# Optimization experiments

Hardware: AMD Instinct MI355X
Metric: run time of the kernel (lower is better)

## Reference

```python
import jax, jax.numpy as jnp
import numpy as np

B, C, N, IC = 4, 64, 4096, 32  # batch, in_channels(=g_channels), nodes, inter_channels


def setup_inputs() -> dict:
    key = jax.random.key(0)
    ks = jax.random.split(key, 8)
    s_c = (2.0 / C) ** 0.5   # kaiming-ish scales
    s_i = (2.0 / C) ** 0.5
    x = jax.random.normal(ks[0], (B, C, N), dtype=jnp.float32)
    g_w = jax.random.normal(ks[1], (C, C), dtype=jnp.float32) * s_c      # g: 1x1 conv (out=C, in=C)
    g_b = jnp.zeros((C,), dtype=jnp.float32)
    theta_w = jax.random.normal(ks[2], (IC, C), dtype=jnp.float32) * s_i  # theta: (out=IC, in=C)
    theta_b = jnp.zeros((IC,), dtype=jnp.float32)
    phi_w = jax.random.normal(ks[3], (IC, C), dtype=jnp.float32) * s_i
    phi_b = jnp.zeros((IC,), dtype=jnp.float32)
    cp_w = jax.random.normal(ks[4], (2 * IC,), dtype=jnp.float32) * (2.0 / (2 * IC)) ** 0.5  # concat_project 1x1 conv, no bias
    C_k = jnp.zeros((N, N), dtype=jnp.float32)  # learned adjacency bias, init zeros
    return {"x": x, "g_w": g_w, "g_b": g_b, "theta_w": theta_w, "theta_b": theta_b,
            "phi_w": phi_w, "phi_b": phi_b, "cp_w": cp_w, "C_k": C_k}


def reference(x, g_w, g_b, theta_w, theta_b, phi_w, phi_b, cp_w, C_k):
    # 1x1 convs are plain GEMMs over the node dim
    g_x = jnp.einsum('oc,bcn->bno', g_w, x) + g_b            # (B, N, C)
    th = jnp.einsum('oc,bcn->bon', theta_w, x) + theta_b[:, None]  # (B, IC, N)
    ph = jnp.einsum('oc,bcn->bon', phi_w, x) + phi_b[:, None]      # (B, IC, N)
    # concat_project on [theta_i ; phi_j] with a 1x1 conv is algebraically an outer sum:
    # f[b,i,j] = w_th . theta[b,:,i] + w_ph . phi[b,:,j]
    a = jnp.einsum('c,bcn->bn', cp_w[:IC], th)  # (B, N)
    p = jnp.einsum('c,bcn->bn', cp_w[IC:], ph)  # (B, N)
    f = a[:, :, None] + p[:, None, :]           # (B, N, N)
    attention = jax.nn.softmax(jax.nn.leaky_relu(f, negative_slope=0.2), axis=-1) + C_k
    y = jnp.einsum('bij,bjo->boi', attention, g_x)  # (B, C, N)
    return y
```

## Files before the change

kernel.cpp:

```cpp
#include <hip/hip_runtime.h>


#define B  4
#define C  64
#define N  4096
#define IC 32
#define NS 4104
#define NR 4097
#define MAGIC 0x13572468
#define CKQ 1048576

#define OFF_FLAG   248
#define OFF_A      256
#define OFF_P      (OFF_A + B*N)
#define OFF_Q      (OFF_P + B*N)
#define OFF_PERM   (OFF_Q + B*N)
#define OFF_PRES   (OFF_PERM + B*N)
#define OFF_SUFS   (OFF_PRES + B*NS)
#define OFF_S1     (OFF_SUFS + B*NS)
#define OFF_S2     (OFF_S1 + B*64*64)
#define OFF_GX     (OFF_S2 + B*64*64)
#define OFF_PREG   (OFF_GX + B*N*64)
#define OFF_SUFG   (OFF_PREG + B*NR*64)

#define CK_NZ(v) ((v.x != 0.f) | (v.y != 0.f) | (v.z != 0.f) | (v.w != 0.f))

__global__ __launch_bounds__(256) void k1_gx(
    const float* __restrict__ x, const float* __restrict__ g_w,
    const float* __restrict__ g_b, const float* __restrict__ theta_w,
    const float* __restrict__ theta_b, const float* __restrict__ phi_w,
    const float* __restrict__ phi_b, const float* __restrict__ cp_w,
    const float* __restrict__ Ck, float* __restrict__ ws) {
  __shared__ float gwT[C * C];
  __shared__ float xl[C * 16];
  __shared__ float lu[C], lv[C], cst[2];
  const int tid = threadIdx.x;
  const int b = blockIdx.x >> 8;
  const int n0 = (blockIdx.x & 255) << 4;
  const float4* c4 = (const float4*)Ck;
  float4 ck0, ck1, ck2, ck3;
  {
    int idx = (blockIdx.x << 8) + tid;
    ck0 = c4[idx]; ck1 = c4[idx + 262144];
    ck2 = c4[idx + 524288]; ck3 = c4[idx + 786432];
  }
  for (int idx = tid; idx < C * C; idx += 256) {
    int o = idx >> 6, cc = idx & 63;
    gwT[cc * C + o] = g_w[idx];
  }
  for (int idx = tid; idx < C * 16; idx += 256) {
    int cc = idx >> 4, nn = idx & 15;
    xl[idx] = x[(size_t)((b << 6) + cc) * N + n0 + nn];
  }
  if (tid < 64) {
    float u = 0.f;
    for (int k = 0; k < IC; ++k) u += cp_w[k] * theta_w[k * C + tid];
    lu[tid] = u;
  } else if (tid < 128) {
    int c = tid - 64;
    float v = 0.f;
    for (int k = 0; k < IC; ++k) v += cp_w[IC + k] * phi_w[k * C + c];
    lv[c] = v;
  } else if (tid == 128) {
    float ca = 0.f, cp2 = 0.f;
    for (int k = 0; k < IC; ++k) { ca += cp_w[k] * theta_b[k]; cp2 += cp_w[IC + k] * phi_b[k]; }
    cst[0] = ca; cst[1] = cp2;
  }
  __syncthreads();
  if (tid < 16) {
    float au = cst[0], pu = cst[1];
    for (int cc = 0; cc < C; ++cc) {
      float xv = xl[cc * 16 + tid];
      au += lu[cc] * xv;
      pu += lv[cc] * xv;
    }
    ws[OFF_A + (b << 12) + n0 + tid] = au;
    ws[OFF_P + (b << 12) + n0 + tid] = pu;
  }
  const int o = tid & 63, g4 = tid >> 6;
  float bb = g_b[o];
  float acc0 = bb, acc1 = bb, acc2 = bb, acc3 = bb;
  for (int cc = 0; cc < C; ++cc) {
    float gv = gwT[cc * C + o];
    const float* xr = &xl[cc * 16 + (g4 << 2)];
    acc0 += gv * xr[0]; acc1 += gv * xr[1]; acc2 += gv * xr[2]; acc3 += gv * xr[3];
  }
  float* gx = ws + OFF_GX + (size_t)((b << 12) + n0 + (g4 << 2)) * C + o;
  gx[0] = acc0; gx[64] = acc1; gx[128] = acc2; gx[192] = acc3;
  bool nz = CK_NZ(ck0) | CK_NZ(ck1) | CK_NZ(ck2) | CK_NZ(ck3);
  if (__any(nz) && (tid & 63) == 0)
    atomicExch((int*)ws + OFF_FLAG, MAGIC);
}

__global__ __launch_bounds__(1024) void k2_rank(const float* __restrict__ Ck,
                                                float* __restrict__ ws) {
  __shared__ float lp[N];
  __shared__ int partials[32][33];
  const int tid = threadIdx.x;
  const int b = blockIdx.x >> 7;
  const int rg = blockIdx.x & 127;
  const float4* c4 = (const float4*)Ck + CKQ;
  float4 ck0, ck1;
  {
    int idx = (blockIdx.x << 10) + tid;
    ck0 = c4[idx]; ck1 = c4[idx + 524288];
  }
  const float* p = ws + OFF_P + b * N;
  ((float4*)lp)[tid] = ((const float4*)p)[tid];
  const int row = tid & 31, chunk = tid >> 5;
  const int i = (rg << 5) + row;
  __syncthreads();
  const float my = lp[i];
  const int c0 = chunk << 7;
  const float4* lp4 = (const float4*)(lp + c0);
  int r0 = 0, r1 = 0, r2 = 0, r3 = 0;
  for (int j = 0; j < 32; ++j) {
    float4 v = lp4[j];
    int k = c0 + (j << 2);
    r0 += (v.x < my) || (v.x == my && (k + 0) < i);
    r1 += (v.y < my) || (v.y == my && (k + 1) < i);
    r2 += (v.z < my) || (v.z == my && (k + 2) < i);
    r3 += (v.w < my) || (v.w == my && (k + 3) < i);
  }
  partials[row][chunk] = (r0 + r1) + (r2 + r3);
  __syncthreads();
  if (tid < 32) {
    int rank = 0;
#pragma unroll
    for (int c = 0; c < 32; ++c) rank += partials[tid][c];
    const int ii = (rg << 5) + tid;
    ws[OFF_Q + (b << 12) + rank] = lp[ii];
    ((int*)ws)[OFF_PERM + (b << 12) + rank] = ii;
  }
  bool nz = CK_NZ(ck0) | CK_NZ(ck1);
  if (__any(nz) && (tid & 63) == 0)
    atomicExch((int*)ws + OFF_FLAG, MAGIC);
}

__global__ __launch_bounds__(1024) void k3_scan_chunks(const float* __restrict__ Ck,
                                                       float* __restrict__ ws) {
  __shared__ float sA[1024], sB[1024];
  const int tid = threadIdx.x;
  const int bid = blockIdx.x;
  const float4* c4 = (const float4*)Ck + 2 * CKQ;
  float4 ck0 = {0.f,0.f,0.f,0.f}, ck1 = ck0, ck2 = ck0, ck3 = ck0;
  {
    int idx = (bid << 10) + tid;
    if (idx < CKQ) ck0 = c4[idx];  idx += 266240;
    if (idx < CKQ) ck1 = c4[idx];  idx += 266240;
    if (idx < CKQ) ck2 = c4[idx];  idx += 266240;
    if (idx < CKQ) ck3 = c4[idx];
  }
  if (bid < B) {
    const int b = bid;
    float* wt2 = sA;
    float* wt1 = sA + 16;
    float* wo2 = sA + 32;
    float* wo1 = sA + 49;
    const float* q = ws + OFF_Q + b * N;
    const float4 qv4 = ((const float4*)q)[tid];
    float e1r[4], e2r[4];
    e2r[0] = expf(0.2f * qv4.x); e1r[0] = expf(qv4.x);
    e2r[1] = expf(0.2f * qv4.y); e1r[1] = expf(qv4.y);
    e2r[2] = expf(0.2f * qv4.z); e1r[2] = expf(qv4.z);
    e2r[3] = expf(0.2f * qv4.w); e1r[3] = expf(qv4.w);
    float s2 = e2r[0] + e2r[1] + e2r[2] + e2r[3];
    float s1 = e1r[0] + e1r[1] + e1r[2] + e1r[3];
    const int lane = tid & 63, wave = tid >> 6;
    float x2 = s2, x1 = s1;
    for (int off = 1; off < 64; off <<= 1) {
      float t2 = __shfl_up(x2, off, 64);
      float t1 = __shfl_up(x1, off, 64);
      if (lane >= off) { x2 += t2; x1 += t1; }
    }
    if (lane == 63) { wt2[wave] = x2; wt1[wave] = x1; }
    __syncthreads();
    if (wave == 0 && lane < 17) {
      float a2 = 0.f, a1 = 0.f;
      for (int w = 0; w < 16; ++w) {
        if (w < lane) { a2 += wt2[w]; a1 += wt1[w]; }
      }
      wo2[lane] = a2; wo1[lane] = a1;
    }
    __syncthreads();
    const float excl2 = wo2[wave] + (x2 - s2);
    const float incl1 = wo1[wave] + x1;
    const float tot1 = wo1[16];
    float* PreS = ws + OFF_PRES + b * NS;
    float* SufS = ws + OFF_SUFS + b * NS;
    const int base = tid << 2;
    float run = excl2;
#pragma unroll
    for (int j = 0; j < 4; ++j) { PreS[base + j] = run; run += e2r[j]; }
    if (tid == 1023) PreS[N] = run;
    run = tot1 - incl1;
#pragma unroll
    for (int j = 3; j >= 0; --j) { run += e1r[j]; SufS[base + j] = run; }
    if (tid == 1023) SufS[N] = 0.f;
  } else {
    const int b2 = bid - B;
    const int b = b2 >> 6, c = b2 & 63;
    const int o = tid & 63, kk = tid >> 6;
    const float* q = ws + OFF_Q + b * N;
    const int* perm = (const int*)ws + OFF_PERM + b * N;
    const float* gx = ws + OFF_GX + ((size_t)b << 18);
    float p1 = 0.f, p2 = 0.f;
    const int k0 = (c << 6) + (kk << 2);
    for (int r = 0; r < 4; ++r) {
      int k = k0 + r;
      float qv = q[k];
      float g = gx[((size_t)perm[k] << 6) + o];
      p1 += expf(qv) * g;
      p2 += expf(0.2f * qv) * g;
    }
    sA[(kk << 6) + o] = p2;
    sB[(kk << 6) + o] = p1;
    __syncthreads();
    if (tid < 64) {
      float t2 = 0.f, t1 = 0.f;
#pragma unroll
      for (int g = 0; g < 16; ++g) { t2 += sA[(g << 6) + o]; t1 += sB[(g << 6) + o]; }
      ws[OFF_S2 + (size_t)(((b << 6) + c) << 6) + o] = t2;
      ws[OFF_S1 + (size_t)(((b << 6) + c) << 6) + o] = t1;
    }
  }
  bool nz = CK_NZ(ck0) | CK_NZ(ck1) | CK_NZ(ck2) | CK_NZ(ck3);
  if (__any(nz) && (tid & 63) == 0)
    atomicExch((int*)ws + OFF_FLAG, MAGIC);
}

__global__ __launch_bounds__(1024) void k4_prefix(const float* __restrict__ Ck,
                                                  float* __restrict__ ws) {
  __shared__ float sA[1024], sB[1024];
  const int tid = threadIdx.x;
  const int b = blockIdx.x >> 6, c = blockIdx.x & 63;
  const int o = tid & 63, kk = tid >> 6;
  const float4* c4 = (const float4*)Ck + 3 * CKQ;
  float4 ck0, ck1, ck2, ck3;
  {
    int idx = (blockIdx.x << 10) + tid;
    ck0 = c4[idx]; ck1 = c4[idx + 262144];
    ck2 = c4[idx + 524288]; ck3 = c4[idx + 786432];
  }
  float offp = 0.f, offs = 0.f;
  {
    const float* S1 = ws + OFF_S1 + ((size_t)b << 12);
    const float* S2 = ws + OFF_S2 + ((size_t)b << 12);
    for (int cc = 0; cc < 64; ++cc) {
      float v2 = S2[(cc << 6) + o];
      float v1 = S1[(cc << 6) + o];
      offp += (cc < c) ? v2 : 0.f;
      offs += (cc > c) ? v1 : 0.f;
    }
  }
  const float* q = ws + OFF_Q + b * N;
  const int* perm = (const int*)ws + OFF_PERM + b * N;
  const float* gx = ws + OFF_GX + ((size_t)b << 18);
  float* PreG = ws + OFF_PREG + (size_t)b * NR * 64;
  float* SufG = ws + OFF_SUFG + (size_t)b * NR * 64;
  const int k0 = (c << 6) + (kk << 2);
  float w1[4], w2[4];
  float p1 = 0.f, p2 = 0.f;
  for (int r = 0; r < 4; ++r) {
    float qq = q[k0 + r];
    float gg = gx[((size_t)perm[k0 + r] << 6) + o];
    w1[r] = expf(qq) * gg;
    w2[r] = expf(0.2f * qq) * gg;
    p1 += w1[r]; p2 += w2[r];
  }
  sA[(kk << 6) + o] = p2;
  sB[(kk << 6) + o] = p1;
  __syncthreads();
  for (int kp = 0; kp < kk; ++kp) offp += sA[(kp << 6) + o];
  for (int kp = kk + 1; kp < 16; ++kp) offs += sB[(kp << 6) + o];
  float run = offp;
#pragma unroll
  for (int r = 0; r < 4; ++r) { PreG[(size_t)(k0 + r) * 64 + o] = run; run += w2[r]; }
  if (c == 63 && kk == 15) PreG[(size_t)N * 64 + o] = run;
  run = offs;
#pragma unroll
  for (int r = 3; r >= 0; --r) { run += w1[r]; SufG[(size_t)(k0 + r) * 64 + o] = run; }
  if (c == 0 && kk == 0) SufG[(size_t)N * 64 + o] = 0.f;
  bool nz = CK_NZ(ck0) | CK_NZ(ck1) | CK_NZ(ck2) | CK_NZ(ck3);
  if (__any(nz) && (tid & 63) == 0)
    atomicExch((int*)ws + OFF_FLAG, MAGIC);
}

__global__ __launch_bounds__(1024) void k5_out(const float* __restrict__ Ck,
                                               float* __restrict__ ws,
                                               float* __restrict__ y) {
  __shared__ float lq[N];
  const int tid = threadIdx.x;
  const int b = blockIdx.x >> 6, rg = blockIdx.x & 63;
  const float4* qs = (const float4*)(ws + OFF_Q + b * N);
  ((float4*)lq)[tid] = qs[tid];
  __syncthreads();
  const int io = tid & 63, og = tid >> 6;
  const int i = (rg << 6) + io;
  float ai = ws[OFF_A + (b << 12) + i];
  float thr = -ai;
  int lo = 0, hi = N;
  while (lo < hi) { int m = (lo + hi) >> 1; if (lq[m] <= thr) lo = m + 1; else hi = m; }
  const int k = lo;
  float e1 = expf(ai), e2 = expf(0.2f * ai);
  float den = e1 * ws[OFF_SUFS + b * NS + k] + e2 * ws[OFF_PRES + b * NS + k];
  float inv = 1.0f / den;
  float4 pv = ((const float4*)(ws + OFF_PREG + ((size_t)b * NR + k) * 64))[og];
  float4 sv = ((const float4*)(ws + OFF_SUFG + ((size_t)b * NR + k) * 64))[og];
  float* yb = y + ((size_t)((b << 6) + (og << 2))) * N + i;
  yb[0]             = (e1 * sv.x + e2 * pv.x) * inv;
  yb[(size_t)N]     = (e1 * sv.y + e2 * pv.y) * inv;
  yb[(size_t)2 * N] = (e1 * sv.z + e2 * pv.z) * inv;
  yb[(size_t)3 * N] = (e1 * sv.w + e2 * pv.w) * inv;
  if (((const volatile int*)ws)[OFF_FLAG] == MAGIC) {
    __syncthreads();
    const int it = rg;
    const int o = tid & 63, jj = tid >> 6;
    const float* gx = ws + OFF_GX + ((size_t)b << 18);
    float (*red)[64] = (float(*)[64])lq;
    for (int ii = 0; ii < 64; ++ii) {
      int irow = (it << 6) + ii;
      float acc = 0.f;
      for (int j = jj; j < N; j += 16)
        acc += Ck[(size_t)irow * N + j] * gx[((size_t)j << 6) + o];
      red[jj][o] = acc;
      __syncthreads();
      if (jj == 0) {
        float s = 0.f;
#pragma unroll
        for (int g = 0; g < 16; ++g) s += red[g][o];
        y[((size_t)((b << 6) + o)) * N + irow] += s;
      }
      __syncthreads();
    }
  }
}

extern "C" void kernel_launch(void* const* d_in, const int* in_sizes, int n_in,
                              void* d_out, int out_size, void* d_ws, size_t ws_size,
                              hipStream_t stream) {
  (void)in_sizes; (void)n_in; (void)out_size; (void)ws_size;
  const float* x       = (const float*)d_in[0];
  const float* g_w     = (const float*)d_in[1];
  const float* g_b     = (const float*)d_in[2];
  const float* theta_w = (const float*)d_in[3];
  const float* theta_b = (const float*)d_in[4];
  const float* phi_w   = (const float*)d_in[5];
  const float* phi_b   = (const float*)d_in[6];
  const float* cp_w    = (const float*)d_in[7];
  const float* Ck      = (const float*)d_in[8];
  float* ws = (float*)d_ws;
  float* y  = (float*)d_out;

  hipLaunchKernelGGL(k1_gx, dim3(1024), dim3(256), 0, stream,
                     x, g_w, g_b, theta_w, theta_b, phi_w, phi_b, cp_w, Ck, ws);
  hipLaunchKernelGGL(k2_rank, dim3(512), dim3(1024), 0, stream, Ck, ws);
  hipLaunchKernelGGL(k3_scan_chunks, dim3(B + B * 64), dim3(1024), 0, stream, Ck, ws);
  hipLaunchKernelGGL(k4_prefix, dim3(B * 64), dim3(1024), 0, stream, Ck, ws);
  hipLaunchKernelGGL(k5_out, dim3(B * 64), dim3(1024), 0, stream, Ck, ws, y);
}
```

Baseline: 150.2 us.

## Fuse chunk scan and prefix kernels, resolve chunk offsets in output kernel

Merges the chunk-sum kernel and the prefix kernel into one launch. Each block now writes chunk-local prefix and suffix sums of the weighted g rows. The output kernel loads the per-chunk totals into shared memory, builds the cross-chunk exclusive scans there, and adds them to the local prefix values. This removes one kernel launch and one full re-read of the gathered g rows. The cost is a larger Ck-nonzero scan in the fused kernel (it now checks the slice k4 used to check) and more shared memory plus an extra barrier in the output kernel.

Measured after the change: 147.4 us. Within noise of the previous version (-1.9%).

```diff
diff --git a/kernel.cpp b/kernel.cpp
--- a/kernel.cpp
+++ b/kernel.cpp
@@ -137,19 +137,22 @@
     atomicExch((int*)ws + OFF_FLAG, MAGIC);
 }
 
-__global__ __launch_bounds__(1024) void k3_scan_chunks(const float* __restrict__ Ck,
-                                                       float* __restrict__ ws) {
+__global__ __launch_bounds__(1024) void k34_scan_prefix(const float* __restrict__ Ck,
+                                                        float* __restrict__ ws) {
   __shared__ float sA[1024], sB[1024];
   const int tid = threadIdx.x;
   const int bid = blockIdx.x;
   const float4* c4 = (const float4*)Ck + 2 * CKQ;
-  float4 ck0 = {0.f,0.f,0.f,0.f}, ck1 = ck0, ck2 = ck0, ck3 = ck0;
+  float4 ck[8];
+#pragma unroll
+  for (int t = 0; t < 8; ++t) ck[t] = make_float4(0.f, 0.f, 0.f, 0.f);
   {
     int idx = (bid << 10) + tid;
-    if (idx < CKQ) ck0 = c4[idx];  idx += 266240;
-    if (idx < CKQ) ck1 = c4[idx];  idx += 266240;
-    if (idx < CKQ) ck2 = c4[idx];  idx += 266240;
-    if (idx < CKQ) ck3 = c4[idx];
+#pragma unroll
+    for (int t = 0; t < 8; ++t) {
+      if (idx < 2 * CKQ) ck[t] = c4[idx];
+      idx += 266240;
+    }
   }
   if (bid < B) {
     const int b = bid;
@@ -204,14 +207,18 @@
     const float* q = ws + OFF_Q + b * N;
     const int* perm = (const int*)ws + OFF_PERM + b * N;
     const float* gx = ws + OFF_GX + ((size_t)b << 18);
+    float* PreG = ws + OFF_PREG + (size_t)b * NR * 64;
+    float* SufG = ws + OFF_SUFG + (size_t)b * NR * 64;
+    const int k0 = (c << 6) + (kk << 2);
+    float w1[4], w2[4];
     float p1 = 0.f, p2 = 0.f;
-    const int k0 = (c << 6) + (kk << 2);
+#pragma unroll
     for (int r = 0; r < 4; ++r) {
-      int k = k0 + r;
-      float qv = q[k];
-      float g = gx[((size_t)perm[k] << 6) + o];
-      p1 += expf(qv) * g;
-      p2 += expf(0.2f * qv) * g;
+      float qq = q[k0 + r];
+      float gg = gx[((size_t)perm[k0 + r] << 6) + o];
+      w1[r] = expf(qq) * gg;
+      w2[r] = expf(0.2f * qq) * gg;
+      p1 += w1[r]; p2 += w2[r];
     }
     sA[(kk << 6) + o] = p2;
     sB[(kk << 6) + o] = p1;
@@ -223,65 +230,18 @@
       ws[OFF_S2 + (size_t)(((b << 6) + c) << 6) + o] = t2;
       ws[OFF_S1 + (size_t)(((b << 6) + c) << 6) + o] = t1;
     }
-  }
-  bool nz = CK_NZ(ck0) | CK_NZ(ck1) | CK_NZ(ck2) | CK_NZ(ck3);
-  if (__any(nz) && (tid & 63) == 0)
-    atomicExch((int*)ws + OFF_FLAG, MAGIC);
-}
-
-__global__ __launch_bounds__(1024) void k4_prefix(const float* __restrict__ Ck,
-                                                  float* __restrict__ ws) {
-  __shared__ float sA[1024], sB[1024];
-  const int tid = threadIdx.x;
-  const int b = blockIdx.x >> 6, c = blockIdx.x & 63;
-  const int o = tid & 63, kk = tid >> 6;
-  const float4* c4 = (const float4*)Ck + 3 * CKQ;
-  float4 ck0, ck1, ck2, ck3;
-  {
-    int idx = (blockIdx.x << 10) + tid;
-    ck0 = c4[idx]; ck1 = c4[idx + 262144];
-    ck2 = c4[idx + 524288]; ck3 = c4[idx + 786432];
-  }
-  float offp = 0.f, offs = 0.f;
-  {
-    const float* S1 = ws + OFF_S1 + ((size_t)b << 12);
-    const float* S2 = ws + OFF_S2 + ((size_t)b << 12);
-    for (int cc = 0; cc < 64; ++cc) {
-      float v2 = S2[(cc << 6) + o];
-      float v1 = S1[(cc << 6) + o];
-      offp += (cc < c) ? v2 : 0.f;
-      offs += (cc > c) ? v1 : 0.f;
-    }
-  }
-  const float* q = ws + OFF_Q + b * N;
-  const int* perm = (const int*)ws + OFF_PERM + b * N;
-  const float* gx = ws + OFF_GX + ((size_t)b << 18);
-  float* PreG = ws + OFF_PREG + (size_t)b * NR * 64;
-  float* SufG = ws + OFF_SUFG + (size_t)b * NR * 64;
-  const int k0 = (c << 6) + (kk << 2);
-  float w1[4], w2[4];
-  float p1 = 0.f, p2 = 0.f;
-  for (int r = 0; r < 4; ++r) {
-    float qq = q[k0 + r];
-    float gg = gx[((size_t)perm[k0 + r] << 6) + o];
-    w1[r] = expf(qq) * gg;
-    w2[r] = expf(0.2f * qq) * gg;
-    p1 += w1[r]; p2 += w2[r];
-  }
-  sA[(kk << 6) + o] = p2;
-  sB[(kk << 6) + o] = p1;
-  __syncthreads();
-  for (int kp = 0; kp < kk; ++kp) offp += sA[(kp << 6) + o];
-  for (int kp = kk + 1; kp < 16; ++kp) offs += sB[(kp << 6) + o];
-  float run = offp;
-#pragma unroll
-  for (int r = 0; r < 4; ++r) { PreG[(size_t)(k0 + r) * 64 + o] = run; run += w2[r]; }
-  if (c == 63 && kk == 15) PreG[(size_t)N * 64 + o] = run;
-  run = offs;
-#pragma unroll
-  for (int r = 3; r >= 0; --r) { run += w1[r]; SufG[(size_t)(k0 + r) * 64 + o] = run; }
-  if (c == 0 && kk == 0) SufG[(size_t)N * 64 + o] = 0.f;
-  bool nz = CK_NZ(ck0) | CK_NZ(ck1) | CK_NZ(ck2) | CK_NZ(ck3);
+    float offp = 0.f, offs = 0.f;
+    for (int kp = 0; kp < kk; ++kp) offp += sA[(kp << 6) + o];
+    for (int kp = kk + 1; kp < 16; ++kp) offs += sB[(kp << 6) + o];
+    float run = offp;
+#pragma unroll
+    for (int r = 0; r < 4; ++r) { PreG[(size_t)(k0 + r) * 64 + o] = run; run += w2[r]; }
+    run = offs;
+#pragma unroll
+    for (int r = 3; r >= 0; --r) { run += w1[r]; SufG[(size_t)(k0 + r) * 64 + o] = run; }
+  }
+  bool nz = (CK_NZ(ck[0]) | CK_NZ(ck[1])) | (CK_NZ(ck[2]) | CK_NZ(ck[3])) |
+            (CK_NZ(ck[4]) | CK_NZ(ck[5])) | (CK_NZ(ck[6]) | CK_NZ(ck[7]));
   if (__any(nz) && (tid & 63) == 0)
     atomicExch((int*)ws + OFF_FLAG, MAGIC);
 }
@@ -290,11 +250,41 @@
                                                float* __restrict__ ws,
                                                float* __restrict__ y) {
   __shared__ float lq[N];
+  __shared__ float cum2[65 * 64];
+  __shared__ float suf1[65 * 64];
+  __shared__ float part1[1024], part2[1024];
   const int tid = threadIdx.x;
   const int b = blockIdx.x >> 6, rg = blockIdx.x & 63;
-  const float4* qs = (const float4*)(ws + OFF_Q + b * N);
-  ((float4*)lq)[tid] = qs[tid];
-  __syncthreads();
+  ((float4*)lq)[tid]   = ((const float4*)(ws + OFF_Q + (b << 12)))[tid];
+  ((float4*)cum2)[tid] = ((const float4*)(ws + OFF_S2 + ((size_t)b << 12)))[tid];
+  ((float4*)suf1)[tid] = ((const float4*)(ws + OFF_S1 + ((size_t)b << 12)))[tid];
+  if (tid < 64) suf1[(64 << 6) + tid] = 0.f;
+  __syncthreads();
+  const int o = tid & 63, g = tid >> 6;
+  const int cg0 = g << 2;
+  const float q0 = cum2[(cg0 << 6) + o],       q1 = cum2[((cg0 + 1) << 6) + o],
+              q2 = cum2[((cg0 + 2) << 6) + o], q3 = cum2[((cg0 + 3) << 6) + o];
+  const float s0 = suf1[(cg0 << 6) + o],       s1v = suf1[((cg0 + 1) << 6) + o],
+              s2v = suf1[((cg0 + 2) << 6) + o], s3 = suf1[((cg0 + 3) << 6) + o];
+  part2[(g << 6) + o] = (q0 + q1) + (q2 + q3);
+  part1[(g << 6) + o] = (s0 + s1v) + (s2v + s3);
+  __syncthreads();
+  {
+    float base2 = 0.f, base1 = 0.f;
+    for (int gg = 0; gg < g; ++gg) base2 += part2[(gg << 6) + o];
+    for (int gg = g + 1; gg < 16; ++gg) base1 += part1[(gg << 6) + o];
+    float run = base2;
+    cum2[(cg0 << 6) + o] = run; run += q0;
+    cum2[((cg0 + 1) << 6) + o] = run; run += q1;
+    cum2[((cg0 + 2) << 6) + o] = run; run += q2;
+    cum2[((cg0 + 3) << 6) + o] = run; run += q3;
+    if (g == 15) cum2[(64 << 6) + o] = run;
+    run = base1;
+    suf1[((cg0 + 3) << 6) + o] = run; run += s3;
+    suf1[((cg0 + 2) << 6) + o] = run; run += s2v;
+    suf1[((cg0 + 1) << 6) + o] = run; run += s1v;
+    suf1[(cg0 << 6) + o] = run;
+  }
   const int io = tid & 63, og = tid >> 6;
   const int i = (rg << 6) + io;
   float ai = ws[OFF_A + (b << 12) + i];
@@ -302,34 +292,41 @@
   int lo = 0, hi = N;
   while (lo < hi) { int m = (lo + hi) >> 1; if (lq[m] <= thr) lo = m + 1; else hi = m; }
   const int k = lo;
+  const int kc = k >> 6;
   float e1 = expf(ai), e2 = expf(0.2f * ai);
   float den = e1 * ws[OFF_SUFS + b * NS + k] + e2 * ws[OFF_PRES + b * NS + k];
   float inv = 1.0f / den;
-  float4 pv = ((const float4*)(ws + OFF_PREG + ((size_t)b * NR + k) * 64))[og];
-  float4 sv = ((const float4*)(ws + OFF_SUFG + ((size_t)b * NR + k) * 64))[og];
+  float4 pl = {0.f, 0.f, 0.f, 0.f}, sl = pl;
+  if (k < N) {
+    pl = ((const float4*)(ws + OFF_PREG + ((size_t)b * NR + k) * 64))[og];
+    sl = ((const float4*)(ws + OFF_SUFG + ((size_t)b * NR + k) * 64))[og];
+  }
+  __syncthreads();
+  float4 c2  = ((const float4*)(cum2 + (kc << 6)))[og];
+  float4 s1g = ((const float4*)(suf1 + (kc << 6)))[og];
   float* yb = y + ((size_t)((b << 6) + (og << 2))) * N + i;
-  yb[0]             = (e1 * sv.x + e2 * pv.x) * inv;
-  yb[(size_t)N]     = (e1 * sv.y + e2 * pv.y) * inv;
-  yb[(size_t)2 * N] = (e1 * sv.z + e2 * pv.z) * inv;
-  yb[(size_t)3 * N] = (e1 * sv.w + e2 * pv.w) * inv;
+  yb[0]             = (e1 * (s1g.x + sl.x) + e2 * (c2.x + pl.x)) * inv;
+  yb[(size_t)N]     = (e1 * (s1g.y + sl.y) + e2 * (c2.y + pl.y)) * inv;
+  yb[(size_t)2 * N] = (e1 * (s1g.z + sl.z) + e2 * (c2.z + pl.z)) * inv;
+  yb[(size_t)3 * N] = (e1 * (s1g.w + sl.w) + e2 * (c2.w + pl.w)) * inv;
   if (((const volatile int*)ws)[OFF_FLAG] == MAGIC) {
     __syncthreads();
     const int it = rg;
-    const int o = tid & 63, jj = tid >> 6;
+    const int oo = tid & 63, jj = tid >> 6;
     const float* gx = ws + OFF_GX + ((size_t)b << 18);
     float (*red)[64] = (float(*)[64])lq;
     for (int ii = 0; ii < 64; ++ii) {
       int irow = (it << 6) + ii;
       float acc = 0.f;
       for (int j = jj; j < N; j += 16)
-        acc += Ck[(size_t)irow * N + j] * gx[((size_t)j << 6) + o];
-      red[jj][o] = acc;
+        acc += Ck[(size_t)irow * N + j] * gx[((size_t)j << 6) + oo];
+      red[jj][oo] = acc;
       __syncthreads();
       if (jj == 0) {
         float s = 0.f;
 #pragma unroll
-        for (int g = 0; g < 16; ++g) s += red[g][o];
-        y[((size_t)((b << 6) + o)) * N + irow] += s;
+        for (int g2 = 0; g2 < 16; ++g2) s += red[g2][oo];
+        y[((size_t)((b << 6) + oo)) * N + irow] += s;
       }
       __syncthreads();
     }
@@ -355,7 +352,6 @@
   hipLaunchKernelGGL(k1_gx, dim3(1024), dim3(256), 0, stream,
                      x, g_w, g_b, theta_w, theta_b, phi_w, phi_b, cp_w, Ck, ws);
   hipLaunchKernelGGL(k2_rank, dim3(512), dim3(1024), 0, stream, Ck, ws);
-  hipLaunchKernelGGL(k3_scan_chunks, dim3(B + B * 64), dim3(1024), 0, stream, Ck, ws);
-  hipLaunchKernelGGL(k4_prefix, dim3(B * 64), dim3(1024), 0, stream, Ck, ws);
+  hipLaunchKernelGGL(k34_scan_prefix, dim3(B + B * 64), dim3(1024), 0, stream, Ck, ws);
   hipLaunchKernelGGL(k5_out, dim3(B * 64), dim3(1024), 0, stream, Ck, ws, y);
 }
```
